# Kernel tuning notes

Measured on AMD Instinct MI355X. Metric: run time of the kernel, lower is better.

## Reference

```python
import jax, jax.numpy as jnp
import numpy as np

IN_DIM = 256
FF = 512
OUT_DIM = 256
BN_EPS = 1e-5


def setup_inputs() -> dict:
    key = jax.random.key(0)
    ks = jax.random.split(key, 9)
    s = lambda k, shape, fan: jax.random.normal(k, shape, dtype=jnp.float32) / np.sqrt(fan)
    return {
        "inputs": jax.random.normal(ks[0], (4, IN_DIM, 16, 16, 16), dtype=jnp.float32),
        "Wk": s(ks[1], (FF, IN_DIM), IN_DIM),
        "bk": jnp.zeros((FF,), jnp.float32),
        "Wq": s(ks[2], (FF, IN_DIM), IN_DIM),
        "bq": jnp.zeros((FF,), jnp.float32),
        "Wv": s(ks[3], (FF, IN_DIM), IN_DIM),
        "bv": jnp.zeros((FF,), jnp.float32),
        "Wo": s(ks[4], (OUT_DIM, FF), FF),
        "bo": jnp.zeros((OUT_DIM,), jnp.float32),
        "gamma": jnp.ones((OUT_DIM,), jnp.float32),
        "beta": jnp.zeros((OUT_DIM,), jnp.float32),
    }


def reference(inputs, Wk, bk, Wq, bq, Wv, bv, Wo, bo, gamma, beta):
    B, Cin, T, H, W = inputs.shape
    # 1x1x1 Conv3d == pointwise channel projection
    proj = lambda Wt, bt: jnp.einsum("oc,bcthw->bothw", Wt, inputs) + bt[None, :, None, None, None]
    K, Q, V = proj(Wk, bk), proj(Wq, bq), proj(Wv, bv)
    C = K.shape[1]
    N = T * H * W
    Kf = K.reshape(B, C, N)
    Qf = Q.reshape(B, C, N)
    Vf = V.reshape(B, C, N)
    # KQ[b,i,j] = sum_c K[b,c,i] Q[b,c,j], scaled by sqrt(in_dim) (per original)
    KQ = jnp.einsum("bci,bcj->bij", Kf, Qf) / jnp.sqrt(jnp.asarray(Cin, jnp.float32))
    attn = jax.nn.softmax(KQ, axis=2)  # (B, N, N)
    # Original: sum_j V[b,c,i] * attn[b,i,j]  ==  V[b,c,i] * rowsum(attn)[b,i]
    # (we avoid materializing the (B,C,N,N) broadcast tensor)
    row = attn.sum(axis=2)  # (B, N), ~1 numerically but kept for faithfulness
    Vagg = (Vf * row[:, None, :]).reshape(B, C, T, H, W)
    V1 = jax.nn.relu(Vagg)
    out = jnp.einsum("oc,bcthw->bothw", Wo, V1) + bo[None, :, None, None, None]
    res = inputs + jax.nn.relu(out)
    # BatchNorm3d in training mode: batch stats over (B, T, H, W) per channel
    mean = res.mean(axis=(0, 2, 3, 4), keepdims=True)
    var = res.var(axis=(0, 2, 3, 4), keepdims=True)
    xhat = (res - mean) * jax.lax.rsqrt(var + BN_EPS)
    return gamma[None, :, None, None, None] * xhat + beta[None, :, None, None, None]
```

## Files before the change

kernel.cpp:

```cpp
#include <hip/hip_runtime.h>

#define NTOT 4096
#define NB   4
#define CIN  256
#define FF   512
#define COUT 256
#define BN_EPS 1e-5f
#define NT_B 32
#define OSP  36

typedef __attribute__((ext_vector_type(8))) short bf16x8;
typedef __attribute__((ext_vector_type(4))) float f32x4;
typedef unsigned short u16;

__device__ __forceinline__ u16 f2bf(float f) {
    unsigned u = __float_as_uint(f);
    u += 0x7fffu + ((u >> 16) & 1u);
    return (u16)(u >> 16);
}
__device__ __forceinline__ float bf2f(u16 h) {
    return __uint_as_float(((unsigned)h) << 16);
}

__global__ __launch_bounds__(256)
void prep_weights(const float* __restrict__ Wv, const float* __restrict__ Wo,
                  u16* __restrict__ Wvh, u16* __restrict__ Wvl,
                  u16* __restrict__ Woh, u16* __restrict__ Wol,
                  float* __restrict__ stats)
{
    const int t = threadIdx.x;
    const int g = blockIdx.x * 256 + t;
    if (blockIdx.x == 0) { stats[t] = 0.f; stats[256 + t] = 0.f; }

    const float* src; u16 *dh, *dl; int m, kg, K;
    if (g < 16384) { m = g >> 5;           kg = g & 31; K = CIN; src = Wv; dh = Wvh; dl = Wvl; }
    else           { int g2 = g - 16384; m = g2 >> 6; kg = g2 & 63; K = FF;  src = Wo; dh = Woh; dl = Wol; }

    const int nkg = K >> 3;
    const size_t gran = ((size_t)(m >> 4) * nkg + kg) * 16 + (m & 15);
    float4 v0 = *(const float4*)&src[(size_t)m * K + kg * 8];
    float4 v1 = *(const float4*)&src[(size_t)m * K + kg * 8 + 4];
    const float f[8] = {v0.x, v0.y, v0.z, v0.w, v1.x, v1.y, v1.z, v1.w};
    u16 h[8], l[8];
    #pragma unroll
    for (int j = 0; j < 8; ++j) { h[j] = f2bf(f[j]); l[j] = f2bf(f[j] - bf2f(h[j])); }
    bf16x8 hv = {(short)h[0],(short)h[1],(short)h[2],(short)h[3],(short)h[4],(short)h[5],(short)h[6],(short)h[7]};
    bf16x8 lv = {(short)l[0],(short)l[1],(short)l[2],(short)l[3],(short)l[4],(short)l[5],(short)l[6],(short)l[7]};
    *(bf16x8*)&dh[gran * 8] = hv;
    *(bf16x8*)&dl[gran * 8] = lv;
}

__global__ __launch_bounds__(256)
void pack_x(const float* __restrict__ x, u16* __restrict__ xh, u16* __restrict__ xl)
{
    __shared__ float xt[CIN][68];
    const int t = threadIdx.x;
    const int b = blockIdx.x >> 6, tb = blockIdx.x & 63;
    const int n0 = tb * 64;
    const int c16 = t >> 4, tok4 = (t & 15) * 4;

    #pragma unroll
    for (int rr = 0; rr < 16; ++rr) {
        const int c = rr * 16 + c16;
        float4 v = *(const float4*)&x[((size_t)b * CIN + c) * NTOT + n0 + tok4];
        *(float4*)&xt[c][tok4] = v;
    }
    __syncthreads();

    const int tok = t & 63, wq = t >> 6;
    const int sb = tok >> 5, tok32 = tok & 31;
    #pragma unroll
    for (int r = 0; r < 8; ++r) {
        const int kg = r * 4 + wq;
        u16 h8[8], l8[8];
        #pragma unroll
        for (int j = 0; j < 8; ++j) {
            float f = xt[kg * 8 + j][tok];
            h8[j] = f2bf(f);
            l8[j] = f2bf(f - bf2f(h8[j]));
        }
        const size_t e = ((((size_t)(b * 128 + tb * 2 + sb)) * 32 + kg) * 32 + tok32) * 8;
        bf16x8 hv = {(short)h8[0],(short)h8[1],(short)h8[2],(short)h8[3],(short)h8[4],(short)h8[5],(short)h8[6],(short)h8[7]};
        bf16x8 lv = {(short)l8[0],(short)l8[1],(short)l8[2],(short)l8[3],(short)l8[4],(short)l8[5],(short)l8[6],(short)l8[7]};
        *(bf16x8*)&xh[e] = hv;
        *(bf16x8*)&xl[e] = lv;
    }
}

__global__ __launch_bounds__(512, 4)
void fused_mlp(const u16* __restrict__ xh, const u16* __restrict__ xl,
               const u16* __restrict__ Wvh, const u16* __restrict__ Wvl,
               const u16* __restrict__ Woh, const u16* __restrict__ Wol,
               const float* __restrict__ bv, const float* __restrict__ bo,
               const float* __restrict__ x, float* __restrict__ out,
               float* __restrict__ stats)
{
    __shared__ __align__(16) unsigned char smem[65536];
    u16*   xsh = (u16*)smem;
    u16*   xsl = (u16*)(smem + 16384);
    u16*   hsh = (u16*)smem;
    u16*   hsl = (u16*)(smem + 32768);
    float* os  = (float*)smem;

    const int t   = threadIdx.x;
    const int b   = blockIdx.x >> 7;
    const int tb2 = blockIdx.x & 127;
    const int n0  = tb2 * NT_B;
    const int ln  = t & 63, w = t >> 6;
    const int l15 = ln & 15, hi = ln >> 4;

    const size_t xbase = ((size_t)(b * 128 + tb2)) * 8192;
    #pragma unroll
    for (int i = 0; i < 2; ++i) {
        const int e = (i * 512 + t) * 8;
        *(bf16x8*)&xsh[e] = *(const bf16x8*)&xh[xbase + e];
        *(bf16x8*)&xsl[e] = *(const bf16x8*)&xl[xbase + e];
    }
    __syncthreads();

    f32x4 acc1[4][2];
    #pragma unroll
    for (int mt = 0; mt < 4; ++mt)
        #pragma unroll
        for (int nt = 0; nt < 2; ++nt)
            acc1[mt][nt] = (f32x4){0.f, 0.f, 0.f, 0.f};

    #pragma unroll 2
    for (int ks = 0; ks < 8; ++ks) {
        bf16x8 bh[2], bl[2];
        #pragma unroll
        for (int nt = 0; nt < 2; ++nt) {
            const int g = (ks * 4 + hi) * 32 + nt * 16 + l15;
            bh[nt] = *(const bf16x8*)&xsh[g * 8];
            bl[nt] = *(const bf16x8*)&xsl[g * 8];
        }
        #pragma unroll
        for (int mt = 0; mt < 4; ++mt) {
            const size_t g = ((size_t)(w * 4 + mt) * 32 + ks * 4 + hi) * 16 + l15;
            bf16x8 ah = *(const bf16x8*)&Wvh[g * 8];
            bf16x8 al = *(const bf16x8*)&Wvl[g * 8];
            #pragma unroll
            for (int nt = 0; nt < 2; ++nt) {
                acc1[mt][nt] = __builtin_amdgcn_mfma_f32_16x16x32_bf16(ah, bh[nt], acc1[mt][nt], 0, 0, 0);
                acc1[mt][nt] = __builtin_amdgcn_mfma_f32_16x16x32_bf16(ah, bl[nt], acc1[mt][nt], 0, 0, 0);
                acc1[mt][nt] = __builtin_amdgcn_mfma_f32_16x16x32_bf16(al, bh[nt], acc1[mt][nt], 0, 0, 0);
            }
        }
    }
    __syncthreads();

    #pragma unroll
    for (int mt = 0; mt < 4; ++mt) {
        const int ff0 = w * 64 + mt * 16 + hi * 4;
        float4 bia = *(const float4*)&bv[ff0];
        const float bb[4] = {bia.x, bia.y, bia.z, bia.w};
        const int kg = ff0 >> 3;
        const int jo = (hi & 1) * 4;
        #pragma unroll
        for (int nt = 0; nt < 2; ++nt) {
            const int tok = nt * 16 + l15;
            u16 hh[4], hl[4];
            #pragma unroll
            for (int r = 0; r < 4; ++r) {
                float v = fmaxf(acc1[mt][nt][r] + bb[r], 0.f);
                hh[r] = f2bf(v);
                hl[r] = f2bf(v - bf2f(hh[r]));
            }
            const int e = (kg * 32 + tok) * 8 + jo;
            *(ushort4*)&hsh[e] = (ushort4){hh[0], hh[1], hh[2], hh[3]};
            *(ushort4*)&hsl[e] = (ushort4){hl[0], hl[1], hl[2], hl[3]};
        }
    }
    __syncthreads();

    f32x4 acc2[2][2];
    #pragma unroll
    for (int mt = 0; mt < 2; ++mt)
        #pragma unroll
        for (int nt = 0; nt < 2; ++nt)
            acc2[mt][nt] = (f32x4){0.f, 0.f, 0.f, 0.f};

    #pragma unroll 2
    for (int ks = 0; ks < 16; ++ks) {
        bf16x8 bh[2], bl[2];
        #pragma unroll
        for (int nt = 0; nt < 2; ++nt) {
            const int g = (ks * 4 + hi) * 32 + nt * 16 + l15;
            bh[nt] = *(const bf16x8*)&hsh[g * 8];
            bl[nt] = *(const bf16x8*)&hsl[g * 8];
        }
        #pragma unroll
        for (int mt = 0; mt < 2; ++mt) {
            const size_t g = ((size_t)(w * 2 + mt) * 64 + ks * 4 + hi) * 16 + l15;
            bf16x8 ah = *(const bf16x8*)&Woh[g * 8];
            bf16x8 al = *(const bf16x8*)&Wol[g * 8];
            #pragma unroll
            for (int nt = 0; nt < 2; ++nt) {
                acc2[mt][nt] = __builtin_amdgcn_mfma_f32_16x16x32_bf16(ah, bh[nt], acc2[mt][nt], 0, 0, 0);
                acc2[mt][nt] = __builtin_amdgcn_mfma_f32_16x16x32_bf16(ah, bl[nt], acc2[mt][nt], 0, 0, 0);
                acc2[mt][nt] = __builtin_amdgcn_mfma_f32_16x16x32_bf16(al, bh[nt], acc2[mt][nt], 0, 0, 0);
            }
        }
    }
    __syncthreads();

    #pragma unroll
    for (int mt = 0; mt < 2; ++mt) {
        const int ch0 = w * 32 + mt * 16 + hi * 4;
        float4 bia = *(const float4*)&bo[ch0];
        const float bb[4] = {bia.x, bia.y, bia.z, bia.w};
        #pragma unroll
        for (int nt = 0; nt < 2; ++nt) {
            const int tok = nt * 16 + l15;
            #pragma unroll
            for (int r = 0; r < 4; ++r)
                os[(ch0 + r) * OSP + tok] = fmaxf(acc2[mt][nt][r] + bb[r], 0.f);
        }
    }
    __syncthreads();

    const int tok4 = (t & 7) * 4;
    const int chb  = t >> 3;
    #pragma unroll
    for (int ii = 0; ii < 4; ++ii) {
        const int ch = chb + ii * 64;
        float4 o = *(float4*)&os[ch * OSP + tok4];
        const size_t goff = ((size_t)b * COUT + ch) * NTOT + n0 + tok4;
        float4 rx = *(const float4*)&x[goff];
        float4 v = {o.x + rx.x, o.y + rx.y, o.z + rx.z, o.w + rx.w};
        *(float4*)&out[goff] = v;
        float s  = v.x + v.y + v.z + v.w;
        float s2 = v.x * v.x + v.y * v.y + v.z * v.z + v.w * v.w;
        #pragma unroll
        for (int off = 1; off < 8; off <<= 1) {
            s  += __shfl_xor(s, off);
            s2 += __shfl_xor(s2, off);
        }
        if ((t & 7) == 0) {
            atomicAdd(&stats[ch], s);
            atomicAdd(&stats[COUT + ch], s2);
        }
    }
}

__global__ __launch_bounds__(256)
void bn_norm(float* __restrict__ out, const float* __restrict__ stats,
             const float* __restrict__ gamma, const float* __restrict__ beta)
{
    const int i4 = blockIdx.x * 256 + threadIdx.x;
    const int c = (i4 >> 10) & (COUT - 1);
    const float inv = 1.0f / (NB * NTOT);
    const float mean = stats[c] * inv;
    const float var  = stats[COUT + c] * inv - mean * mean;
    const float sc = gamma[c] * rsqrtf(var + BN_EPS);
    const float sh = beta[c] - mean * sc;
    float4 v = reinterpret_cast<float4*>(out)[i4];
    v.x = v.x * sc + sh;
    v.y = v.y * sc + sh;
    v.z = v.z * sc + sh;
    v.w = v.w * sc + sh;
    reinterpret_cast<float4*>(out)[i4] = v;
}

extern "C" void kernel_launch(void* const* d_in, const int* in_sizes, int n_in,
                              void* d_out, int out_size, void* d_ws, size_t ws_size,
                              hipStream_t stream)
{
    const float* x     = (const float*)d_in[0];
    const float* Wv    = (const float*)d_in[5];
    const float* bv    = (const float*)d_in[6];
    const float* Wo    = (const float*)d_in[7];
    const float* bo    = (const float*)d_in[8];
    const float* gamma = (const float*)d_in[9];
    const float* beta  = (const float*)d_in[10];
    float* out = (float*)d_out;

    u16* xh   = (u16*)d_ws;
    u16* xl   = xh  + (size_t)NB * NTOT * CIN;
    u16* Wvh  = xl  + (size_t)NB * NTOT * CIN;
    u16* Wvl  = Wvh + (size_t)FF * CIN;
    u16* Woh  = Wvl + (size_t)FF * CIN;
    u16* Wol  = Woh + (size_t)COUT * FF;
    float* stats = (float*)(Wol + (size_t)COUT * FF);

    prep_weights<<<128, 256, 0, stream>>>(Wv, Wo, Wvh, Wvl, Woh, Wol, stats);
    pack_x<<<NB * 64, 256, 0, stream>>>(x, xh, xl);
    fused_mlp<<<NB * 128, 512, 0, stream>>>(xh, xl, Wvh, Wvl, Woh, Wol,
                                            bv, bo, x, out, stats);
    bn_norm<<<(NB * COUT * NTOT / 4) / 256, 256, 0, stream>>>(out, stats, gamma, beta);
}
```

Baseline: 160.2 us.

## Software-pipeline weight and LDS operand loads in both MFMA GEMM loops

Both GEMM loops are fully unrolled and double-buffered, so the global weight fragments and LDS activation fragments for the next k-step load while the MFMAs for the current step run. The first weight load is issued before the barrier that follows the x staging, and the first Wo load before the barrier ahead of stage two, to hide global latency. This raises register pressure from the extra fragment buffers and larger unrolled code, which could lower occupancy.

```diff
diff --git a/kernel.cpp b/kernel.cpp
--- a/kernel.cpp
+++ b/kernel.cpp
@@ -13,6 +13,8 @@
 typedef __attribute__((ext_vector_type(4))) float f32x4;
 typedef unsigned short u16;
 
+#define MFMA16(A, B, C) __builtin_amdgcn_mfma_f32_16x16x32_bf16((A), (B), (C), 0, 0, 0)
+
 __device__ __forceinline__ u16 f2bf(float f) {
     unsigned u = __float_as_uint(f);
     u += 0x7fffu + ((u >> 16) & 1u);
@@ -116,7 +118,6 @@
         *(bf16x8*)&xsh[e] = *(const bf16x8*)&xh[xbase + e];
         *(bf16x8*)&xsl[e] = *(const bf16x8*)&xl[xbase + e];
     }
-    __syncthreads();
 
     f32x4 acc1[4][2];
     #pragma unroll
@@ -125,28 +126,80 @@
         for (int nt = 0; nt < 2; ++nt)
             acc1[mt][nt] = (f32x4){0.f, 0.f, 0.f, 0.f};
 
-    #pragma unroll 2
-    for (int ks = 0; ks < 8; ++ks) {
-        bf16x8 bh[2], bl[2];
-        #pragma unroll
-        for (int nt = 0; nt < 2; ++nt) {
-            const int g = (ks * 4 + hi) * 32 + nt * 16 + l15;
-            bh[nt] = *(const bf16x8*)&xsh[g * 8];
-            bl[nt] = *(const bf16x8*)&xsl[g * 8];
-        }
-        #pragma unroll
-        for (int mt = 0; mt < 4; ++mt) {
-            const size_t g = ((size_t)(w * 4 + mt) * 32 + ks * 4 + hi) * 16 + l15;
-            bf16x8 ah = *(const bf16x8*)&Wvh[g * 8];
-            bf16x8 al = *(const bf16x8*)&Wvl[g * 8];
-            #pragma unroll
-            for (int nt = 0; nt < 2; ++nt) {
-                acc1[mt][nt] = __builtin_amdgcn_mfma_f32_16x16x32_bf16(ah, bh[nt], acc1[mt][nt], 0, 0, 0);
-                acc1[mt][nt] = __builtin_amdgcn_mfma_f32_16x16x32_bf16(ah, bl[nt], acc1[mt][nt], 0, 0, 0);
-                acc1[mt][nt] = __builtin_amdgcn_mfma_f32_16x16x32_bf16(al, bh[nt], acc1[mt][nt], 0, 0, 0);
-            }
-        }
-    }
+#define LDW1(KS, P, WH, WL) do { _Pragma("unroll")                              \
+    for (int i_ = 0; i_ < 2; ++i_) {                                            \
+        const int mt_ = (P) * 2 + i_;                                           \
+        const size_t g_ = ((size_t)(w * 4 + mt_) * 32 + (KS) * 4 + hi) * 16 + l15; \
+        WH[i_] = *(const bf16x8*)&Wvh[g_ * 8];                                  \
+        WL[i_] = *(const bf16x8*)&Wvl[g_ * 8];                                  \
+    } } while (0)
+#define LDB1(KS, BH, BL) do { _Pragma("unroll")                                 \
+    for (int nt_ = 0; nt_ < 2; ++nt_) {                                         \
+        const int g_ = ((KS) * 4 + hi) * 32 + nt_ * 16 + l15;                   \
+        BH[nt_] = *(const bf16x8*)&xsh[g_ * 8];                                 \
+        BL[nt_] = *(const bf16x8*)&xsl[g_ * 8];                                 \
+    } } while (0)
+#define MM1(P, WH, WL, BH, BL) do { _Pragma("unroll")                           \
+    for (int i_ = 0; i_ < 2; ++i_) { _Pragma("unroll")                          \
+        for (int nt_ = 0; nt_ < 2; ++nt_) {                                     \
+            acc1[(P)*2+i_][nt_] = MFMA16(WH[i_], BH[nt_], acc1[(P)*2+i_][nt_]); \
+            acc1[(P)*2+i_][nt_] = MFMA16(WH[i_], BL[nt_], acc1[(P)*2+i_][nt_]); \
+            acc1[(P)*2+i_][nt_] = MFMA16(WL[i_], BH[nt_], acc1[(P)*2+i_][nt_]); \
+    } } } while (0)
+
+    bf16x8 w1hA[2], w1lA[2], w1hB[2], w1lB[2];
+    bf16x8 b1hE[2], b1lE[2], b1hO[2], b1lO[2];
+
+    LDW1(0, 0, w1hA, w1lA);
+    __syncthreads();
+    LDB1(0, b1hE, b1lE);
+
+    #pragma unroll
+    for (int s = 0; s < 16; ++s) {
+        const int ks = s >> 1, p = s & 1;
+        if (p == 0) {
+            LDW1(ks, 1, w1hB, w1lB);
+        } else if (ks < 7) {
+            LDW1(ks + 1, 0, w1hA, w1lA);
+            if (ks & 1) { LDB1(ks + 1, b1hE, b1lE); }
+            else        { LDB1(ks + 1, b1hO, b1lO); }
+        }
+        if (p == 0) {
+            if (ks & 1) MM1(0, w1hA, w1lA, b1hO, b1lO);
+            else        MM1(0, w1hA, w1lA, b1hE, b1lE);
+        } else {
+            if (ks & 1) MM1(1, w1hB, w1lB, b1hO, b1lO);
+            else        MM1(1, w1hB, w1lB, b1hE, b1lE);
+        }
+    }
+#undef LDW1
+#undef LDB1
+#undef MM1
+
+#define LDW2(KS, WH, WL) do { _Pragma("unroll")                                 \
+    for (int mt_ = 0; mt_ < 2; ++mt_) {                                         \
+        const size_t g_ = ((size_t)(w * 2 + mt_) * 64 + (KS) * 4 + hi) * 16 + l15; \
+        WH[mt_] = *(const bf16x8*)&Woh[g_ * 8];                                 \
+        WL[mt_] = *(const bf16x8*)&Wol[g_ * 8];                                 \
+    } } while (0)
+#define LDB2(KS, BH, BL) do { _Pragma("unroll")                                 \
+    for (int nt_ = 0; nt_ < 2; ++nt_) {                                         \
+        const int g_ = ((KS) * 4 + hi) * 32 + nt_ * 16 + l15;                   \
+        BH[nt_] = *(const bf16x8*)&hsh[g_ * 8];                                 \
+        BL[nt_] = *(const bf16x8*)&hsl[g_ * 8];                                 \
+    } } while (0)
+#define MM2(WH, WL, BH, BL) do { _Pragma("unroll")                              \
+    for (int mt_ = 0; mt_ < 2; ++mt_) { _Pragma("unroll")                       \
+        for (int nt_ = 0; nt_ < 2; ++nt_) {                                     \
+            acc2[mt_][nt_] = MFMA16(WH[mt_], BH[nt_], acc2[mt_][nt_]);          \
+            acc2[mt_][nt_] = MFMA16(WH[mt_], BL[nt_], acc2[mt_][nt_]);          \
+            acc2[mt_][nt_] = MFMA16(WL[mt_], BH[nt_], acc2[mt_][nt_]);          \
+    } } } while (0)
+
+    bf16x8 w2hA[2], w2lA[2], w2hB[2], w2lB[2];
+    bf16x8 b2hE[2], b2lE[2], b2hO[2], b2lO[2];
+    LDW2(0, w2hA, w2lA);
+
     __syncthreads();
 
     #pragma unroll
@@ -180,28 +233,20 @@
         for (int nt = 0; nt < 2; ++nt)
             acc2[mt][nt] = (f32x4){0.f, 0.f, 0.f, 0.f};
 
-    #pragma unroll 2
+    LDB2(0, b2hE, b2lE);
+    #pragma unroll
     for (int ks = 0; ks < 16; ++ks) {
-        bf16x8 bh[2], bl[2];
-        #pragma unroll
-        for (int nt = 0; nt < 2; ++nt) {
-            const int g = (ks * 4 + hi) * 32 + nt * 16 + l15;
-            bh[nt] = *(const bf16x8*)&hsh[g * 8];
-            bl[nt] = *(const bf16x8*)&hsl[g * 8];
-        }
-        #pragma unroll
-        for (int mt = 0; mt < 2; ++mt) {
-            const size_t g = ((size_t)(w * 2 + mt) * 64 + ks * 4 + hi) * 16 + l15;
-            bf16x8 ah = *(const bf16x8*)&Woh[g * 8];
-            bf16x8 al = *(const bf16x8*)&Wol[g * 8];
-            #pragma unroll
-            for (int nt = 0; nt < 2; ++nt) {
-                acc2[mt][nt] = __builtin_amdgcn_mfma_f32_16x16x32_bf16(ah, bh[nt], acc2[mt][nt], 0, 0, 0);
-                acc2[mt][nt] = __builtin_amdgcn_mfma_f32_16x16x32_bf16(ah, bl[nt], acc2[mt][nt], 0, 0, 0);
-                acc2[mt][nt] = __builtin_amdgcn_mfma_f32_16x16x32_bf16(al, bh[nt], acc2[mt][nt], 0, 0, 0);
-            }
-        }
-    }
+        if (ks < 15) {
+            if (ks & 1) { LDW2(ks + 1, w2hA, w2lA); LDB2(ks + 1, b2hE, b2lE); }
+            else        { LDW2(ks + 1, w2hB, w2lB); LDB2(ks + 1, b2hO, b2lO); }
+        }
+        if (ks & 1) MM2(w2hB, w2lB, b2hO, b2lO);
+        else        MM2(w2hA, w2lA, b2hE, b2lE);
+    }
+#undef LDW2
+#undef LDB2
+#undef MM2
+
     __syncthreads();
 
     #pragma unroll
```

After: 159.0 us. About the same (-0.8%).
